# Kernel tuning notes

Hardware: AMD Instinct MI355X
Metric: run time of the kernel (lower is better)

The kernel has to match this reference:

```python
import jax, jax.numpy as jnp
import numpy as np

N_NODES = 100000
N_EDGES = 1600000
IN_CH = 128
OUT_CH = 64
NEG_SLOPE = 0.2
EPS = 1e-10


def setup_inputs() -> dict:
    key = jax.random.key(0)
    k1, k2, k3, k4, k5 = jax.random.split(key, 5)
    x = jax.random.normal(k1, (N_NODES, IN_CH), dtype=jnp.float32)
    edge_index = jax.random.randint(k2, (2, N_EDGES), 0, N_NODES, dtype=jnp.int64)
    W = jax.random.normal(k3, (OUT_CH, IN_CH), dtype=jnp.float32) * (1.0 / np.sqrt(IN_CH))
    a_l = jax.random.normal(k4, (OUT_CH,), dtype=jnp.float32) * (1.0 / np.sqrt(OUT_CH))
    a_r = jax.random.normal(k5, (OUT_CH,), dtype=jnp.float32) * (1.0 / np.sqrt(OUT_CH))
    bias = jnp.zeros((OUT_CH,), dtype=jnp.float32)
    return {"x": x, "edge_index": edge_index, "W": W, "a_l": a_l, "a_r": a_r, "bias": bias}


def reference(x, edge_index, W, a_l, a_r, bias):
    N = x.shape[0]
    h = x @ W.T                     # (N, out_ch)
    src, dst = edge_index[0], edge_index[1]
    e_l = h @ a_l                   # (N,)
    e_r = h @ a_r                   # (N,)
    edge_attn = jax.nn.leaky_relu(e_l[dst] + e_r[src], negative_slope=NEG_SLOPE)  # (E,)
    # segment softmax over incoming edges of each dst node
    edge_max = jax.ops.segment_max(edge_attn, dst, num_segments=N)  # (N,), -inf for isolated
    edge_attn = jnp.exp(edge_attn - edge_max[dst])
    edge_sum = jax.ops.segment_sum(edge_attn, dst, num_segments=N)  # (N,)
    edge_attn = edge_attn / (edge_sum[dst] + EPS)
    messages = h[src] * edge_attn[:, None]                          # (E, out_ch)
    out = jax.ops.segment_sum(messages, dst, num_segments=N)        # (N, out_ch)
    return out + bias
```

## Files before the change

### kernel.cpp

```cpp
#include <hip/hip_runtime.h>
#include <math.h>

#define NN 100000
#define NE 1600000
#define IC 128
#define OC 64
#define NEG_SLOPE 0.2f
#define EPS_F 1e-10f

#define NSLICE 500
#define SN 200
#define EB 500
#define QPB 800
#define CAP 3600
#define SLEN (NSLICE * EB)

typedef short bf16x8 __attribute__((ext_vector_type(8)));
typedef float f32x4 __attribute__((ext_vector_type(4)));

__device__ __forceinline__ unsigned short f2bf(float f) {
    unsigned u = __float_as_uint(f);
    u += 0x7fff + ((u >> 16) & 1);
    return (unsigned short)(u >> 16);
}

__global__ __launch_bounds__(256) void linear_kernel(
    const float* __restrict__ x, const float* __restrict__ W,
    const float* __restrict__ a_l, const float* __restrict__ a_r,
    unsigned short* __restrict__ h_bf, float* __restrict__ e_l,
    float* __restrict__ e_r)
{
    __shared__ unsigned short lds[128 * 136];
    const int tid = threadIdx.x;
    const int n0 = blockIdx.x * 64;

#pragma unroll
    for (int it = 0; it < 8; it++) {
        int i = it * 256 + tid;
        int r = i >> 5, c4 = i & 31;
        int n = n0 + r;
        float4 v = make_float4(0.f, 0.f, 0.f, 0.f);
        if (n < NN) v = *(const float4*)&x[(size_t)n * 128 + (c4 << 2)];
        ushort4 b;
        b.x = f2bf(v.x); b.y = f2bf(v.y); b.z = f2bf(v.z); b.w = f2bf(v.w);
        *(ushort4*)&lds[r * 136 + (c4 << 2)] = b;
    }
#pragma unroll
    for (int it = 0; it < 8; it++) {
        int i = it * 256 + tid;
        int r = i >> 5, c4 = i & 31;
        float4 v = *(const float4*)&W[r * 128 + (c4 << 2)];
        ushort4 b;
        b.x = f2bf(v.x); b.y = f2bf(v.y); b.z = f2bf(v.z); b.w = f2bf(v.w);
        *(ushort4*)&lds[(64 + r) * 136 + (c4 << 2)] = b;
    }
    __syncthreads();

    const int wv = tid >> 6;
    const int lane = tid & 63;
    const int q = lane >> 4;
    const int c = lane & 15;

    f32x4 acc[4];
#pragma unroll
    for (int t = 0; t < 4; t++) acc[t] = (f32x4){0.f, 0.f, 0.f, 0.f};

    const unsigned short* xrow = &lds[(wv * 16 + c) * 136];
    const unsigned short* wrow = &lds[(64 + c) * 136];

#pragma unroll
    for (int kk = 0; kk < 4; kk++) {
        int ko = kk * 32 + q * 8;
        bf16x8 a = *(const bf16x8*)&xrow[ko];
#pragma unroll
        for (int t = 0; t < 4; t++) {
            bf16x8 b = *(const bf16x8*)&wrow[t * 16 * 136 + ko];
            acc[t] = __builtin_amdgcn_mfma_f32_16x16x32_bf16(a, b, acc[t], 0, 0, 0);
        }
    }

#pragma unroll
    for (int r = 0; r < 4; r++) {
        int m = n0 + wv * 16 + q * 4 + r;
        if (m < NN) {
#pragma unroll
            for (int t = 0; t < 4; t++)
                h_bf[(size_t)m * OC + t * 16 + c] = f2bf(acc[t][r]);
        }
    }

    float al[4], ar[4];
#pragma unroll
    for (int t = 0; t < 4; t++) { al[t] = a_l[t * 16 + c]; ar[t] = a_r[t * 16 + c]; }
    float pl[4], pr[4];
#pragma unroll
    for (int r = 0; r < 4; r++) {
        pl[r] = al[0] * acc[0][r] + al[1] * acc[1][r] + al[2] * acc[2][r] + al[3] * acc[3][r];
        pr[r] = ar[0] * acc[0][r] + ar[1] * acc[1][r] + ar[2] * acc[2][r] + ar[3] * acc[3][r];
    }
#pragma unroll
    for (int m = 1; m < 16; m <<= 1) {
#pragma unroll
        for (int r = 0; r < 4; r++) {
            pl[r] += __shfl_xor(pl[r], m);
            pr[r] += __shfl_xor(pr[r], m);
        }
    }
    if (c == 0) {
#pragma unroll
        for (int r = 0; r < 4; r++) {
            int m = n0 + wv * 16 + q * 4 + r;
            if (m < NN) { e_l[m] = pl[r]; e_r[m] = pr[r]; }
        }
    }
}

__global__ __launch_bounds__(256) void hist_kernel(
    const int* __restrict__ dst, int* __restrict__ H)
{
    __shared__ int hist[NSLICE];
    const int t = threadIdx.x, b = blockIdx.x;
    for (int i = t; i < NSLICE; i += 256) hist[i] = 0;
    __syncthreads();
    for (int qi = t; qi < QPB; qi += 256) {
        int4 d = ((const int4*)dst)[b * QPB + qi];
        atomicAdd(&hist[d.x / SN], 1);
        atomicAdd(&hist[d.y / SN], 1);
        atomicAdd(&hist[d.z / SN], 1);
        atomicAdd(&hist[d.w / SN], 1);
    }
    __syncthreads();
    for (int i = t; i < NSLICE; i += 256) H[i * EB + b] = hist[i];
}

__global__ __launch_bounds__(1024) void scan_block_kernel(
    const int* __restrict__ deg, int* __restrict__ offsets,
    int* __restrict__ bsums)
{
    __shared__ int wsum[16];
    const int t = threadIdx.x;
    const int lane = t & 63, wv = t >> 6;
    const int i = blockIdx.x * 1024 + t;
    int v = (i < SLEN) ? deg[i] : 0;
    int incl = v;
#pragma unroll
    for (int off = 1; off < 64; off <<= 1) {
        int u = __shfl_up(incl, off);
        if (lane >= off) incl += u;
    }
    if (lane == 63) wsum[wv] = incl;
    __syncthreads();
    if (wv == 0 && lane < 16) {
        int s = wsum[lane];
        int si = s;
#pragma unroll
        for (int off = 1; off < 16; off <<= 1) {
            int u = __shfl_up(si, off);
            if (lane >= off) si += u;
        }
        wsum[lane] = si - s;
    }
    __syncthreads();
    int excl = incl - v + wsum[wv];
    if (i < SLEN) offsets[i] = excl;
    if (t == 1023) bsums[blockIdx.x] = excl + v;
}

__global__ __launch_bounds__(256) void scan_bsums_kernel(int* __restrict__ bsums)
{
    __shared__ int s[256];
    const int t = threadIdx.x;
    const int NB = (SLEN + 1023) / 1024;
    int v = (t < NB) ? bsums[t] : 0;
    s[t] = v;
    __syncthreads();
    for (int off = 1; off < 256; off <<= 1) {
        int u = (t >= off) ? s[t - off] : 0;
        __syncthreads();
        s[t] += u;
        __syncthreads();
    }
    if (t < NB) bsums[t] = s[t] - v;
}

__global__ __launch_bounds__(256) void bucket_kernel(
    const int* __restrict__ src, const int* __restrict__ dst,
    const int* __restrict__ O_raw, const int* __restrict__ bsums,
    int* __restrict__ bucketed)
{
    __shared__ int cur[NSLICE];
    const int t = threadIdx.x, b = blockIdx.x;
    for (int i = t; i < NSLICE; i += 256) {
        int gi = i * EB + b;
        cur[i] = O_raw[gi] + bsums[gi >> 10];
    }
    __syncthreads();
    for (int qi = t; qi < QPB; qi += 256) {
        int4 d4 = ((const int4*)dst)[b * QPB + qi];
        int4 s4 = ((const int4*)src)[b * QPB + qi];
        int dd[4] = {d4.x, d4.y, d4.z, d4.w};
        int ss[4] = {s4.x, s4.y, s4.z, s4.w};
#pragma unroll
        for (int k = 0; k < 4; k++) {
            int sl = dd[k] / SN;
            int pos = atomicAdd(&cur[sl], 1);
            bucketed[pos] = ((dd[k] - sl * SN) << 17) | ss[k];
        }
    }
}

__global__ __launch_bounds__(1024, 8) void fused_sort_agg_kernel(
    const int* __restrict__ bucketed, const int* __restrict__ O_raw,
    const int* __restrict__ bsums, const float* __restrict__ e_l,
    const float* __restrict__ e_r, const unsigned short* __restrict__ h_bf,
    const float* __restrict__ bias, float* __restrict__ out)
{
    __shared__ int2 sorted[CAP];
    __shared__ int hist[SN];
    __shared__ float nsum[SN];
    __shared__ float el[SN];
    __shared__ int wsums[4];

    const int s = blockIdx.x, t = threadIdx.x;
    int gi0 = s * EB;
    const int B0 = O_raw[gi0] + bsums[gi0 >> 10];
    int B1 = NE;
    if (s < NSLICE - 1) {
        int gi1 = (s + 1) * EB;
        B1 = O_raw[gi1] + bsums[gi1 >> 10];
    }
    int cnt = B1 - B0;
    if (cnt > CAP) cnt = CAP;

    if (t < SN) {
        hist[t] = 0;
        nsum[t] = 0.f;
        el[t] = e_l[s * SN + t];
    }
    __syncthreads();

    int pr[4]; float wr[4];
#pragma unroll
    for (int k = 0; k < 4; k++) {
        int i = t + k * 1024;
        if (i < cnt) {
            int p = __builtin_nontemporal_load(&bucketed[B0 + i]);
            int dloc = p >> 17;
            float a = el[dloc] + e_r[p & 0x1FFFF];
            a = (a > 0.f) ? a : NEG_SLOPE * a;
            float w = __expf(a);
            pr[k] = p; wr[k] = w;
            atomicAdd(&hist[dloc], 1);
            atomicAdd(&nsum[dloc], w);
        }
    }
    __syncthreads();

    const int lane = t & 63, w4 = t >> 6;
    int v = (t < SN) ? hist[t] : 0;
    int incl = v;
#pragma unroll
    for (int o = 1; o < 64; o <<= 1) {
        int u = __shfl_up(incl, o);
        if (lane >= o) incl += u;
    }
    if (w4 < 4 && lane == 63) wsums[w4] = incl;
    __syncthreads();
    if (t == 0) {
        int run = 0;
#pragma unroll
        for (int k = 0; k < 4; k++) { int x = wsums[k]; wsums[k] = run; run += x; }
    }
    __syncthreads();
    int excl = incl - v + ((w4 < 4) ? wsums[w4] : 0);
    if (t < SN) hist[t] = excl;
    __syncthreads();

#pragma unroll
    for (int k = 0; k < 4; k++) {
        int i = t + k * 1024;
        if (i < cnt) {
            int dloc = pr[k] >> 17;
            int pos = atomicAdd(&hist[dloc], 1);
            sorted[pos] = make_int2(pr[k] & 0x1FFFF, __float_as_int(wr[k]));
        }
    }
    __syncthreads();

    const int wv = t >> 6;
    const int grp = lane >> 3;
    const int ch = (lane & 7) * 8;
    float4 bb0 = make_float4(0.f, 0.f, 0.f, 0.f), bb1 = bb0;
    if (lane < 8) {
        bb0 = *(const float4*)&bias[lane * 8];
        bb1 = *(const float4*)&bias[lane * 8 + 4];
    }

    for (int n = wv; n < SN; n += 16) {
        int start = (n == 0) ? 0 : hist[n - 1];
        int end = hist[n];
        float acc[8] = {0.f, 0.f, 0.f, 0.f, 0.f, 0.f, 0.f, 0.f};

#pragma unroll 2
        for (int j = start; j < end; j += 8) {
            int eidx = j + grp;
            int ej = (eidx < end) ? eidx : end - 1;
            int2 p = sorted[ej];
            float w = (eidx < end) ? __int_as_float(p.y) : 0.f;
            uint4 qv = *(const uint4*)&h_bf[(size_t)p.x * OC + ch];
            acc[0] += w * __uint_as_float(qv.x << 16);
            acc[1] += w * __uint_as_float(qv.x & 0xffff0000u);
            acc[2] += w * __uint_as_float(qv.y << 16);
            acc[3] += w * __uint_as_float(qv.y & 0xffff0000u);
            acc[4] += w * __uint_as_float(qv.z << 16);
            acc[5] += w * __uint_as_float(qv.z & 0xffff0000u);
            acc[6] += w * __uint_as_float(qv.w << 16);
            acc[7] += w * __uint_as_float(qv.w & 0xffff0000u);
        }

#pragma unroll
        for (int m = 8; m <= 32; m <<= 1) {
#pragma unroll
            for (int k = 0; k < 8; k++) acc[k] += __shfl_xor(acc[k], m);
        }

        if (lane < 8) {
            float rinv = 1.0f / (nsum[n] + EPS_F);
            int node = s * SN + n;
            f32x4 o0 = { acc[0] * rinv + bb0.x, acc[1] * rinv + bb0.y,
                         acc[2] * rinv + bb0.z, acc[3] * rinv + bb0.w };
            f32x4 o1 = { acc[4] * rinv + bb1.x, acc[5] * rinv + bb1.y,
                         acc[6] * rinv + bb1.z, acc[7] * rinv + bb1.w };
            __builtin_nontemporal_store(o0, (f32x4*)&out[(size_t)node * OC + lane * 8]);
            __builtin_nontemporal_store(o1, (f32x4*)&out[(size_t)node * OC + lane * 8 + 4]);
        }
    }
}

extern "C" void kernel_launch(void* const* d_in, const int* in_sizes, int n_in,
                              void* d_out, int out_size, void* d_ws, size_t ws_size,
                              hipStream_t stream)
{
    const float* x = (const float*)d_in[0];
    const int* edge_index = (const int*)d_in[1];
    const float* W = (const float*)d_in[2];
    const float* a_l = (const float*)d_in[3];
    const float* a_r = (const float*)d_in[4];
    const float* bias = (const float*)d_in[5];
    float* out = (float*)d_out;

    const int* src = edge_index;
    const int* dst = edge_index + NE;

    char* w = (char*)d_ws;
    unsigned short* h_bf = (unsigned short*)w;
    size_t off = (size_t)NN * OC * 2;
    float* e_l = (float*)(w + off); off += (size_t)NN * 4;
    float* e_r = (float*)(w + off); off += (size_t)NN * 4;
    int* H = (int*)(w + off);       off += (size_t)SLEN * 4;
    int* O_raw = (int*)(w + off);   off += (size_t)(SLEN + 4) * 4;
    int* bsums = (int*)(w + off);   off += 256 * 4;
    int* bucketed = (int*)(w + off); off += (size_t)NE * 4;

    linear_kernel<<<(NN + 63) / 64, 256, 0, stream>>>(x, W, a_l, a_r, h_bf, e_l, e_r);
    hist_kernel<<<EB, 256, 0, stream>>>(dst, H);
    scan_block_kernel<<<(SLEN + 1023) / 1024, 1024, 0, stream>>>(H, O_raw, bsums);
    scan_bsums_kernel<<<1, 256, 0, stream>>>(bsums);
    bucket_kernel<<<EB, 256, 0, stream>>>(src, dst, O_raw, bsums, bucketed);
    fused_sort_agg_kernel<<<NSLICE, 1024, 0, stream>>>(bucketed, O_raw, bsums, e_l, e_r,
                                                       h_bf, bias, out);
}
```

Baseline: 190.7 us.

## Aggregate each node with an 8-lane group and compute softmax denominator inline

The aggregation phase now gives each destination node to an 8-thread group, where it was a full 64-lane wavefront before. Each group walks that node's edges serially, unrolled by 4, so the cross-lane xor-shuffle reduction disappears. The per-node weight sum is accumulated in registers during aggregation, which removes the shared nsum array and its float atomicAdds. The cost is less parallelism per node: a high-degree node takes more serial iterations and lanes within a wave are load-imbalanced.

```diff
diff --git a/kernel.cpp b/kernel.cpp
--- a/kernel.cpp
+++ b/kernel.cpp
@@ -217,7 +217,6 @@
 {
     __shared__ int2 sorted[CAP];
     __shared__ int hist[SN];
-    __shared__ float nsum[SN];
     __shared__ float el[SN];
     __shared__ int wsums[4];
 
@@ -234,7 +233,6 @@
 
     if (t < SN) {
         hist[t] = 0;
-        nsum[t] = 0.f;
         el[t] = e_l[s * SN + t];
     }
     __syncthreads();
@@ -251,7 +249,6 @@
             float w = __expf(a);
             pr[k] = p; wr[k] = w;
             atomicAdd(&hist[dloc], 1);
-            atomicAdd(&nsum[dloc], w);
         }
     }
     __syncthreads();
@@ -287,53 +284,46 @@
     }
     __syncthreads();
 
-    const int wv = t >> 6;
-    const int grp = lane >> 3;
-    const int ch = (lane & 7) * 8;
-    float4 bb0 = make_float4(0.f, 0.f, 0.f, 0.f), bb1 = bb0;
-    if (lane < 8) {
-        bb0 = *(const float4*)&bias[lane * 8];
-        bb1 = *(const float4*)&bias[lane * 8 + 4];
-    }
-
-    for (int n = wv; n < SN; n += 16) {
-        int start = (n == 0) ? 0 : hist[n - 1];
-        int end = hist[n];
+    const int g = t >> 3;
+    const int ch = (t & 7) * 8;
+    float4 bb0 = *(const float4*)&bias[ch];
+    float4 bb1 = *(const float4*)&bias[ch + 4];
+
+    for (int n = g; n < SN; n += 128) {
+        const int start = (n == 0) ? 0 : hist[n - 1];
+        const int end = hist[n];
         float acc[8] = {0.f, 0.f, 0.f, 0.f, 0.f, 0.f, 0.f, 0.f};
-
-#pragma unroll 2
-        for (int j = start; j < end; j += 8) {
-            int eidx = j + grp;
-            int ej = (eidx < end) ? eidx : end - 1;
-            int2 p = sorted[ej];
-            float w = (eidx < end) ? __int_as_float(p.y) : 0.f;
-            uint4 qv = *(const uint4*)&h_bf[(size_t)p.x * OC + ch];
-            acc[0] += w * __uint_as_float(qv.x << 16);
-            acc[1] += w * __uint_as_float(qv.x & 0xffff0000u);
-            acc[2] += w * __uint_as_float(qv.y << 16);
-            acc[3] += w * __uint_as_float(qv.y & 0xffff0000u);
-            acc[4] += w * __uint_as_float(qv.z << 16);
-            acc[5] += w * __uint_as_float(qv.z & 0xffff0000u);
-            acc[6] += w * __uint_as_float(qv.w << 16);
-            acc[7] += w * __uint_as_float(qv.w & 0xffff0000u);
-        }
-
-#pragma unroll
-        for (int m = 8; m <= 32; m <<= 1) {
-#pragma unroll
-            for (int k = 0; k < 8; k++) acc[k] += __shfl_xor(acc[k], m);
-        }
-
-        if (lane < 8) {
-            float rinv = 1.0f / (nsum[n] + EPS_F);
-            int node = s * SN + n;
-            f32x4 o0 = { acc[0] * rinv + bb0.x, acc[1] * rinv + bb0.y,
-                         acc[2] * rinv + bb0.z, acc[3] * rinv + bb0.w };
-            f32x4 o1 = { acc[4] * rinv + bb1.x, acc[5] * rinv + bb1.y,
-                         acc[6] * rinv + bb1.z, acc[7] * rinv + bb1.w };
-            __builtin_nontemporal_store(o0, (f32x4*)&out[(size_t)node * OC + lane * 8]);
-            __builtin_nontemporal_store(o1, (f32x4*)&out[(size_t)node * OC + lane * 8 + 4]);
-        }
+        float ws = 0.f;
+
+        for (int j = start; j < end; j += 4) {
+#pragma unroll
+            for (int u = 0; u < 4; u++) {
+                int e = j + u;
+                int ec = (e < end) ? e : (end - 1);
+                int2 p = sorted[ec];
+                float w = (e < end) ? __int_as_float(p.y) : 0.f;
+                const unsigned short* hp = h_bf + (((unsigned)p.x << 6) + ch);
+                uint4 qv = *(const uint4*)hp;
+                ws += w;
+                acc[0] += w * __uint_as_float(qv.x << 16);
+                acc[1] += w * __uint_as_float(qv.x & 0xffff0000u);
+                acc[2] += w * __uint_as_float(qv.y << 16);
+                acc[3] += w * __uint_as_float(qv.y & 0xffff0000u);
+                acc[4] += w * __uint_as_float(qv.z << 16);
+                acc[5] += w * __uint_as_float(qv.z & 0xffff0000u);
+                acc[6] += w * __uint_as_float(qv.w << 16);
+                acc[7] += w * __uint_as_float(qv.w & 0xffff0000u);
+            }
+        }
+
+        float rinv = 1.0f / (ws + EPS_F);
+        int node = s * SN + n;
+        f32x4 o0 = { acc[0] * rinv + bb0.x, acc[1] * rinv + bb0.y,
+                     acc[2] * rinv + bb0.z, acc[3] * rinv + bb0.w };
+        f32x4 o1 = { acc[4] * rinv + bb1.x, acc[5] * rinv + bb1.y,
+                     acc[6] * rinv + bb1.z, acc[7] * rinv + bb1.w };
+        __builtin_nontemporal_store(o0, (f32x4*)&out[(size_t)node * OC + ch]);
+        __builtin_nontemporal_store(o1, (f32x4*)&out[(size_t)node * OC + ch + 4]);
     }
 }
 
```

Measured after the change: 175.4 us. 1.09x faster.
